# Optimization experiments

Measured on AMD Instinct MI355X. Metric: run time of the kernel, lower is better.

## Reference

```python
import jax, jax.numpy as jnp
import numpy as np

B, S, D, H = 8, 1024, 1024, 16
HD = D // H  # head_size = 64


def layernorm(x, g, b, eps=1e-5):
    mu = jnp.mean(x, axis=-1, keepdims=True)
    var = jnp.var(x, axis=-1, keepdims=True)
    return (x - mu) * jax.lax.rsqrt(var + eps) * g + b


def setup_inputs() -> dict:
    key = jax.random.key(0)
    ks = jax.random.split(key, 12)
    s_attn = 1.0 / np.sqrt(D)
    inp = {
        "x": jax.random.normal(ks[0], (B, S, D), dtype=jnp.float32),
        # per-head q/k/v projections (bias=False), stacked: [H, D, HD]
        "Wq": jax.random.normal(ks[1], (H, D, HD), dtype=jnp.float32) * s_attn,
        "Wk": jax.random.normal(ks[2], (H, D, HD), dtype=jnp.float32) * s_attn,
        "Wv": jax.random.normal(ks[3], (H, D, HD), dtype=jnp.float32) * s_attn,
        "Wo": jax.random.normal(ks[4], (D, D), dtype=jnp.float32) * s_attn,
        "bo": jnp.zeros((D,), dtype=jnp.float32),
        # FFN: hidden = 1 * n_embd (as in source)
        "W1": jax.random.normal(ks[5], (D, D), dtype=jnp.float32) * s_attn,
        "b1": jnp.zeros((D,), dtype=jnp.float32),
        "W2": jax.random.normal(ks[6], (D, D), dtype=jnp.float32) * s_attn,
        "b2": jnp.zeros((D,), dtype=jnp.float32),
        "g_ln1": jnp.ones((D,), dtype=jnp.float32),
        "b_ln1": jnp.zeros((D,), dtype=jnp.float32),
        "g_ln2": jnp.ones((D,), dtype=jnp.float32),
        "b_ln2": jnp.zeros((D,), dtype=jnp.float32),
    }
    return inp


def reference(x, Wq, Wk, Wv, Wo, bo, W1, b1, W2, b2, g_ln1, b_ln1, g_ln2, b_ln2):
    # pre-LN self-attention
    h = layernorm(x, g_ln1, b_ln1)
    q = jnp.einsum("bsd,hde->bhse", h, Wq)
    k = jnp.einsum("bsd,hde->bhse", h, Wk)
    v = jnp.einsum("bsd,hde->bhse", h, Wv)
    scale = HD ** -0.5  # k.shape[-1] ** -0.5
    wei = jax.nn.softmax(jnp.einsum("bhse,bhte->bhst", q, k) * scale, axis=-1)
    attn = jnp.einsum("bhst,bhte->bhse", wei, v)  # [B,H,S,HD]
    # concat heads (head order matches torch.cat over head list)
    attn = attn.transpose(0, 2, 1, 3).reshape(B, S, D)
    sa = attn @ Wo + bo
    x = x + sa
    # pre-LN FFN with exact GELU (torch nn.GELU default)
    h2 = layernorm(x, g_ln2, b_ln2)
    ff = jax.nn.gelu(h2 @ W1 + b1, approximate=False) @ W2 + b2
    return x + ff
```

## Files before the change

kernel.cpp:

```cpp
#include <hip/hip_runtime.h>
#include <hip/hip_bf16.h>
#include <math.h>

#define B_ 8
#define S_ 1024
#define D_ 1024
#define H_ 16
#define HD_ 64

typedef __bf16 bf16x8 __attribute__((ext_vector_type(8)));
typedef __bf16 bf16x4 __attribute__((ext_vector_type(4)));
typedef float f32x4 __attribute__((ext_vector_type(4)));

__device__ __forceinline__ void gld_lds16(const __bf16* g, __bf16* l) {
  __builtin_amdgcn_global_load_lds(
      (const __attribute__((address_space(1))) void*)g,
      (__attribute__((address_space(3))) void*)l, 16, 0, 0);
}

__global__ __launch_bounds__(256) void ln_kernel(const float* __restrict__ x,
                                                 const float* __restrict__ g,
                                                 const float* __restrict__ b,
                                                 __bf16* __restrict__ out) {
  int row = blockIdx.x;
  const float* xr = x + (size_t)row * D_;
  __bf16* outr = out + (size_t)row * D_;
  int tid = threadIdx.x;

  float4 v = ((const float4*)xr)[tid];
  float s = v.x + v.y + v.z + v.w;
  float ss = v.x * v.x + v.y * v.y + v.z * v.z + v.w * v.w;

  #pragma unroll
  for (int m = 1; m < 64; m <<= 1) {
    s += __shfl_xor(s, m);
    ss += __shfl_xor(ss, m);
  }
  __shared__ float red[10];
  int wid = tid >> 6;
  if ((tid & 63) == 0) { red[wid] = s; red[4 + wid] = ss; }
  __syncthreads();
  if (tid == 0) {
    float ts = red[0] + red[1] + red[2] + red[3];
    float tss = red[4] + red[5] + red[6] + red[7];
    float mu = ts * (1.0f / D_);
    float var = tss * (1.0f / D_) - mu * mu;
    red[8] = mu;
    red[9] = rsqrtf(var + 1e-5f);
  }
  __syncthreads();
  float mu = red[8], rstd = red[9];
  float4 gv = ((const float4*)g)[tid];
  float4 bv = ((const float4*)b)[tid];
  bf16x4 o;
  o[0] = (__bf16)((v.x - mu) * rstd * gv.x + bv.x);
  o[1] = (__bf16)((v.y - mu) * rstd * gv.y + bv.y);
  o[2] = (__bf16)((v.z - mu) * rstd * gv.z + bv.z);
  o[3] = (__bf16)((v.w - mu) * rstd * gv.w + bv.w);
  *(bf16x4*)(outr + tid * 4) = o;
}

__global__ __launch_bounds__(256) void transpose_w(const float* __restrict__ in,
                                                   __bf16* __restrict__ out) {
  __shared__ float t[64][65];
  const int n0 = blockIdx.x * 64, k0 = blockIdx.y * 64;
  const int tid = threadIdx.x;
  const int r = tid >> 4, c4 = (tid & 15) * 4;
  #pragma unroll
  for (int i = 0; i < 4; ++i) {
    float4 v = *(const float4*)&in[(size_t)(k0 + i * 16 + r) * D_ + n0 + c4];
    t[i * 16 + r][c4 + 0] = v.x;
    t[i * 16 + r][c4 + 1] = v.y;
    t[i * 16 + r][c4 + 2] = v.z;
    t[i * 16 + r][c4 + 3] = v.w;
  }
  __syncthreads();
  #pragma unroll
  for (int i = 0; i < 4; ++i) {
    bf16x4 o;
    #pragma unroll
    for (int j = 0; j < 4; ++j) o[j] = (__bf16)t[c4 + j][i * 16 + r];
    *(bf16x4*)&out[(size_t)(n0 + i * 16 + r) * D_ + k0 + c4] = o;
  }
}

__global__ __launch_bounds__(256) void transpose_qkv(const float* __restrict__ Wq,
                                                     const float* __restrict__ Wk,
                                                     const float* __restrict__ Wv,
                                                     __bf16* __restrict__ out) {
  __shared__ float t[64][65];
  const int d0 = blockIdx.x * 64;
  const int h = blockIdx.y;
  const int which = blockIdx.z;
  const float* in = (which == 0 ? Wq : which == 1 ? Wk : Wv) + (size_t)h * D_ * HD_;
  const int tid = threadIdx.x;
  const int r = tid >> 4, c4 = (tid & 15) * 4;
  #pragma unroll
  for (int i = 0; i < 4; ++i) {
    float4 v = *(const float4*)&in[(size_t)(d0 + i * 16 + r) * HD_ + c4];
    t[i * 16 + r][c4 + 0] = v.x;
    t[i * 16 + r][c4 + 1] = v.y;
    t[i * 16 + r][c4 + 2] = v.z;
    t[i * 16 + r][c4 + 3] = v.w;
  }
  __syncthreads();
  #pragma unroll
  for (int i = 0; i < 4; ++i) {
    bf16x4 o;
    #pragma unroll
    for (int j = 0; j < 4; ++j) o[j] = (__bf16)t[c4 + j][i * 16 + r];
    *(bf16x4*)&out[(size_t)(which * 1024 + h * 64 + i * 16 + r) * D_ + d0 + c4] = o;
  }
}

#define MODE_QKV 0
#define MODE_PROJ 1
#define MODE_FF1 2
#define MODE_FF2 3

template <int MODE>
__global__ __launch_bounds__(256) void gemm_mfma(const __bf16* __restrict__ A,
                                                 const __bf16* __restrict__ Bt,
                                                 const float* __restrict__ bias,
                                                 const float* __restrict__ resid,
                                                 float* __restrict__ outf,
                                                 __bf16* __restrict__ outb,
                                                 int M, int N, int K) {
  __shared__ __align__(16) __bf16 As[128 * 64];
  __shared__ __align__(16) __bf16 Bs[128 * 64];
  const int tid = threadIdx.x;

  const int gx = (int)gridDim.x;
  const int nwg = gx * (int)gridDim.y;
  const int flat = (int)blockIdx.y * gx + (int)blockIdx.x;
  const int wg = (flat & 7) * (nwg >> 3) + (flat >> 3);
  const int m0 = (wg / gx) * 128, n0 = (wg % gx) * 128;

  const int w = tid >> 6, l = tid & 63, lr = l & 15, lg = l >> 4;
  const int wm = (w >> 1) * 64, wn = (w & 1) * 64;

  f32x4 acc[4][4] = {};

  for (int k0 = 0; k0 < K; k0 += 64) {
    __syncthreads();
    #pragma unroll
    for (int i = 0; i < 4; ++i) {
      int e = i * 256 + tid;
      int row = e >> 3;
      int col = ((e & 7) ^ (row & 7)) * 8;
      gld_lds16(A + (size_t)(m0 + row) * K + k0 + col, &As[e * 8]);
    }
    #pragma unroll
    for (int i = 0; i < 4; ++i) {
      int e = i * 256 + tid;
      int row = e >> 3;
      int col = ((e & 7) ^ (row & 7)) * 8;
      gld_lds16(Bt + (size_t)(n0 + row) * K + k0 + col, &Bs[e * 8]);
    }
    asm volatile("s_waitcnt vmcnt(0)");
    __syncthreads();

    #pragma unroll
    for (int kk = 0; kk < 2; ++kk) {
      bf16x8 af[4], bfr[4];
      #pragma unroll
      for (int i = 0; i < 4; ++i)
        af[i] = *(const bf16x8*)
            &As[((wm + i * 16 + lr) * 8 + ((kk * 4 + lg) ^ (lr & 7))) * 8];
      #pragma unroll
      for (int j = 0; j < 4; ++j)
        bfr[j] = *(const bf16x8*)
            &Bs[((wn + j * 16 + lr) * 8 + ((kk * 4 + lg) ^ (lr & 7))) * 8];
      #pragma unroll
      for (int i = 0; i < 4; ++i)
        #pragma unroll
        for (int j = 0; j < 4; ++j)
          acc[i][j] = __builtin_amdgcn_mfma_f32_16x16x32_bf16(af[i], bfr[j], acc[i][j], 0, 0, 0);
    }
  }

  #pragma unroll
  for (int i = 0; i < 4; ++i) {
    #pragma unroll
    for (int j = 0; j < 4; ++j) {
      #pragma unroll
      for (int r = 0; r < 4; ++r) {
        int m = m0 + wm + i * 16 + 4 * lg + r;
        int n = n0 + wn + j * 16 + lr;
        float val = acc[i][j][r];
        if (MODE == MODE_QKV) {
          int b = m >> 10, s = m & 1023;
          int which = n >> 10, hh = (n >> 6) & 15, e = n & 63;
          outb[(size_t)which * 8388608 + ((size_t)(b * 16 + hh) * 1024 + s) * 64 + e] =
              (__bf16)val;
        } else if (MODE == MODE_PROJ) {
          size_t idx = (size_t)m * 1024 + n;
          outf[idx] = resid[idx] + val + bias[n];
        } else if (MODE == MODE_FF1) {
          val += bias[n];
          outb[(size_t)m * 1024 + n] =
              (__bf16)(0.5f * val * (1.0f + erff(val * 0.70710678118654752f)));
        } else {
          size_t idx = (size_t)m * 1024 + n;
          outf[idx] = outf[idx] + val + bias[n];
        }
      }
    }
  }
}

__global__ __launch_bounds__(512) void fattn(const __bf16* __restrict__ q,
                                             const __bf16* __restrict__ k,
                                             const __bf16* __restrict__ v,
                                             __bf16* __restrict__ outC) {
  __shared__ __align__(16) __bf16 Klds[2][64 * 64];
  __shared__ __align__(16) __bf16 Vp[2][64][72];

  const int bid = blockIdx.x;
  const int bh = (bid & 7) * 16 + ((bid >> 3) & 15);
  const int qt = bid >> 7;
  const int tid = threadIdx.x;
  const int w = tid >> 6, l = tid & 63;
  const int lr = l & 15, lg = l >> 4;

  const size_t base = (size_t)bh * (S_ * HD_);
  const int qrow0 = qt * 128 + w * 16;
  const __bf16* kg = k + base;
  const __bf16* vg = v + base;

  const int krow = tid >> 3;
  const int kcol = ((tid & 7) ^ (krow & 7)) * 8;
  const int vc = (l & 0x20) + ((l & 0xC) << 1) + ((l & 0x10) >> 2) + (l & 3);

  bf16x8 qf0, qf1;
  {
    const __bf16* qp = q + base + (size_t)(qrow0 + lr) * HD_ + lg * 8;
    qf0 = *(const bf16x8*)(qp);
    qf1 = *(const bf16x8*)(qp + 32);
    #pragma unroll
    for (int i = 0; i < 8; ++i) qf0[i] = (__bf16)((float)qf0[i] * 0.125f);
    #pragma unroll
    for (int i = 0; i < 8; ++i) qf1[i] = (__bf16)((float)qf1[i] * 0.125f);
  }

  f32x4 oacc[4] = {{0,0,0,0},{0,0,0,0},{0,0,0,0},{0,0,0,0}};
  float m_run = -1e30f, l_run = 0.f;

  gld_lds16(kg + (size_t)krow * HD_ + kcol, &Klds[0][tid * 8]);
  bf16x8 vr0, vr1;
  if (w < 4) {
    const __bf16* vp = vg + (size_t)l * HD_ + w * 16;
    vr0 = *(const bf16x8*)vp;
    vr1 = *(const bf16x8*)(vp + 8);
    #pragma unroll
    for (int i = 0; i < 8; ++i) Vp[0][w * 16 + i][vc] = vr0[i];
    #pragma unroll
    for (int i = 0; i < 8; ++i) Vp[0][w * 16 + 8 + i][vc] = vr1[i];
    const __bf16* vp1 = vg + (size_t)(64 + l) * HD_ + w * 16;
    vr0 = *(const bf16x8*)vp1;
    vr1 = *(const bf16x8*)(vp1 + 8);
  }
  asm volatile("s_waitcnt vmcnt(0)");
  __syncthreads();

  int cur = 0;
  for (int t = 0; t < 16; ++t) {
    {
      int tn = (t < 15) ? (t + 1) : 15;
      gld_lds16(kg + ((size_t)tn * 64 + krow) * HD_ + kcol, &Klds[cur ^ 1][tid * 8]);
    }

    f32x4 sacc[4];
    const __bf16* kb = &Klds[cur][0];
    __builtin_amdgcn_s_setprio(1);
    #pragma unroll
    for (int g = 0; g < 4; ++g) {
      bf16x8 kf0 = *(const bf16x8*)&kb[((16 * g + lr) * 8 + (lg ^ (lr & 7))) * 8];
      bf16x8 kf1 = *(const bf16x8*)&kb[((16 * g + lr) * 8 + ((lg + 4) ^ (lr & 7))) * 8];
      f32x4 z = {0.f, 0.f, 0.f, 0.f};
      z = __builtin_amdgcn_mfma_f32_16x16x32_bf16(kf0, qf0, z, 0, 0, 0);
      sacc[g] = __builtin_amdgcn_mfma_f32_16x16x32_bf16(kf1, qf1, z, 0, 0, 0);
    }
    __builtin_amdgcn_s_setprio(0);

    float tm = sacc[0][0];
    #pragma unroll
    for (int g = 0; g < 4; ++g)
      #pragma unroll
      for (int r = 0; r < 4; ++r) tm = fmaxf(tm, sacc[g][r]);
    tm = fmaxf(tm, __shfl_xor(tm, 16));
    tm = fmaxf(tm, __shfl_xor(tm, 32));

    if (!__all(tm - m_run <= 8.0f)) {
      float mn = fmaxf(m_run, tm);
      float corr = __expf(m_run - mn);
      m_run = mn;
      l_run *= corr;
      #pragma unroll
      for (int r = 0; r < 4; ++r) {
        float cq = __shfl(corr, 4 * lg + r);
        #pragma unroll
        for (int g = 0; g < 4; ++g) oacc[g][r] *= cq;
      }
    }

    float p[4][4];
    float ps = 0.f;
    #pragma unroll
    for (int g = 0; g < 4; ++g)
      #pragma unroll
      for (int r = 0; r < 4; ++r) {
        p[g][r] = __expf(sacc[g][r] - m_run);
        ps += p[g][r];
      }
    ps += __shfl_xor(ps, 16);
    ps += __shfl_xor(ps, 32);
    l_run += ps;

    if (w < 4) {
      #pragma unroll
      for (int i = 0; i < 8; ++i) Vp[cur ^ 1][w * 16 + i][vc] = vr0[i];
      #pragma unroll
      for (int i = 0; i < 8; ++i) Vp[cur ^ 1][w * 16 + 8 + i][vc] = vr1[i];
      int tnn = (t < 14) ? (t + 2) : 15;
      const __bf16* vp = vg + ((size_t)tnn * 64 + l) * HD_ + w * 16;
      vr0 = *(const bf16x8*)vp;
      vr1 = *(const bf16x8*)(vp + 8);
    }

    bf16x8 af0, af1;
    #pragma unroll
    for (int j = 0; j < 8; ++j) {
      af0[j] = (__bf16)p[j >> 2][j & 3];
      af1[j] = (__bf16)p[2 + (j >> 2)][j & 3];
    }
    __builtin_amdgcn_s_setprio(1);
    #pragma unroll
    for (int g = 0; g < 4; ++g) {
      bf16x8 vf0 = *(const bf16x8*)&Vp[cur][16 * g + lr][lg * 8];
      bf16x8 vf1 = *(const bf16x8*)&Vp[cur][16 * g + lr][32 + lg * 8];
      oacc[g] = __builtin_amdgcn_mfma_f32_16x16x32_bf16(af0, vf0, oacc[g], 0, 0, 0);
      oacc[g] = __builtin_amdgcn_mfma_f32_16x16x32_bf16(af1, vf1, oacc[g], 0, 0, 0);
    }
    __builtin_amdgcn_s_setprio(0);

    asm volatile("s_waitcnt vmcnt(0)");
    __syncthreads();
    cur ^= 1;
  }

  const int b = bh >> 4, hh = bh & 15;
  #pragma unroll
  for (int r = 0; r < 4; ++r) {
    float linv = 1.0f / __shfl(l_run, 4 * lg + r);
    int srow = qrow0 + 4 * lg + r;
    __bf16* op = outC + ((size_t)(b * S_ + srow)) * D_ + hh * HD_;
    #pragma unroll
    for (int g = 0; g < 4; ++g) op[16 * g + lr] = (__bf16)(oacc[g][r] * linv);
  }
}

extern "C" void kernel_launch(void* const* d_in, const int* in_sizes, int n_in,
                              void* d_out, int out_size, void* d_ws, size_t ws_size,
                              hipStream_t stream) {
  const float* x   = (const float*)d_in[0];
  const float* Wq  = (const float*)d_in[1];
  const float* Wk  = (const float*)d_in[2];
  const float* Wv  = (const float*)d_in[3];
  const float* Wo  = (const float*)d_in[4];
  const float* bo  = (const float*)d_in[5];
  const float* W1  = (const float*)d_in[6];
  const float* b1  = (const float*)d_in[7];
  const float* W2  = (const float*)d_in[8];
  const float* b2  = (const float*)d_in[9];
  const float* g1  = (const float*)d_in[10];
  const float* bl1 = (const float*)d_in[11];
  const float* g2  = (const float*)d_in[12];
  const float* bl2 = (const float*)d_in[13];
  float* out = (float*)d_out;

  const size_t MN = (size_t)B_ * S_ * D_;
  __bf16* h     = (__bf16*)d_ws;
  __bf16* wt    = h + MN;
  __bf16* qkv   = wt + (size_t)6144 * 1024;
  __bf16* attnC = qkv + 3 * MN;
  __bf16* ff1   = attnC + MN;

  __bf16* wqkv_t = wt;
  __bf16* wo_t   = wt + (size_t)3072 * 1024;
  __bf16* w1_t   = wt + (size_t)4096 * 1024;
  __bf16* w2_t   = wt + (size_t)5120 * 1024;

  const int rows = B_ * S_;

  ln_kernel<<<rows, 256, 0, stream>>>(x, g1, bl1, h);
  transpose_qkv<<<dim3(16, 16, 3), 256, 0, stream>>>(Wq, Wk, Wv, wqkv_t);
  transpose_w<<<dim3(16, 16), 256, 0, stream>>>(Wo, wo_t);
  transpose_w<<<dim3(16, 16), 256, 0, stream>>>(W1, w1_t);
  transpose_w<<<dim3(16, 16), 256, 0, stream>>>(W2, w2_t);

  gemm_mfma<MODE_QKV><<<dim3(24, 64), 256, 0, stream>>>(
      h, wqkv_t, nullptr, nullptr, nullptr, qkv, rows, 3072, D_);
  fattn<<<1024, 512, 0, stream>>>(qkv, qkv + MN, qkv + 2 * MN, attnC);
  gemm_mfma<MODE_PROJ><<<dim3(8, 64), 256, 0, stream>>>(
      attnC, wo_t, bo, x, out, nullptr, rows, D_, D_);
  ln_kernel<<<rows, 256, 0, stream>>>(out, g2, bl2, h);
  gemm_mfma<MODE_FF1><<<dim3(8, 64), 256, 0, stream>>>(
      h, w1_t, b1, nullptr, nullptr, ff1, rows, D_, D_);
  gemm_mfma<MODE_FF2><<<dim3(8, 64), 256, 0, stream>>>(
      ff1, w2_t, b2, nullptr, out, nullptr, rows, D_, D_);
}
```

Measured before the change: 254.4 us.

## Merge weight transposes, fold softmax scale into QKV, compute row sums via MFMA

Replaces four weight-transpose launches with a single kernel over six matrices. The attention scale and log2(e) are folded into the Q projection epilogue so the attention kernel can use exp2f and skip rescaling Q. The softmax denominator now comes from an extra MFMA against a ones vector instead of shuffle reductions, and the rescale threshold is raised. V staging uses all 8 waves with an XOR-swizzled LDS layout instead of a padded one, which removes a register buffer. These cut launch overhead and VALU/shuffle work in the attention loop, at the cost of two extra MFMAs per tile and the row sum being built from bf16-rounded probabilities.

```diff
diff --git a/kernel.cpp b/kernel.cpp
--- a/kernel.cpp
+++ b/kernel.cpp
@@ -11,6 +11,8 @@
 typedef __bf16 bf16x8 __attribute__((ext_vector_type(8)));
 typedef __bf16 bf16x4 __attribute__((ext_vector_type(4)));
 typedef float f32x4 __attribute__((ext_vector_type(4)));
+
+#define FMAX3(a, b, c) fmaxf(fmaxf((a), (b)), (c))
 
 __device__ __forceinline__ void gld_lds16(const __bf16* g, __bf16* l) {
   __builtin_amdgcn_global_load_lds(
@@ -60,15 +62,37 @@
   *(bf16x4*)(outr + tid * 4) = o;
 }
 
-__global__ __launch_bounds__(256) void transpose_w(const float* __restrict__ in,
-                                                   __bf16* __restrict__ out) {
+__global__ __launch_bounds__(256) void transpose_all(const float* __restrict__ Wq,
+                                                     const float* __restrict__ Wk,
+                                                     const float* __restrict__ Wv,
+                                                     const float* __restrict__ Wo,
+                                                     const float* __restrict__ W1,
+                                                     const float* __restrict__ W2,
+                                                     __bf16* __restrict__ out) {
   __shared__ float t[64][65];
-  const int n0 = blockIdx.x * 64, k0 = blockIdx.y * 64;
+  const int x = blockIdx.x, y = blockIdx.y, z = blockIdx.z;
   const int tid = threadIdx.x;
   const int r = tid >> 4, c4 = (tid & 15) * 4;
+
+  const float* src;
+  int stride, orowbase, kbase;
+  if (z < 3) {
+    const float* W = (z == 0 ? Wq : z == 1 ? Wk : Wv);
+    src = W + (size_t)y * (D_ * HD_) + (size_t)(x * 64) * HD_;
+    stride = HD_;
+    orowbase = z * 1024 + y * 64;
+    kbase = x * 64;
+  } else {
+    const float* W = (z == 3 ? Wo : z == 4 ? W1 : W2);
+    src = W + (size_t)(y * 64) * D_ + x * 64;
+    stride = D_;
+    orowbase = z * 1024 + x * 64;
+    kbase = y * 64;
+  }
+
   #pragma unroll
   for (int i = 0; i < 4; ++i) {
-    float4 v = *(const float4*)&in[(size_t)(k0 + i * 16 + r) * D_ + n0 + c4];
+    float4 v = *(const float4*)&src[(size_t)(i * 16 + r) * stride + c4];
     t[i * 16 + r][c4 + 0] = v.x;
     t[i * 16 + r][c4 + 1] = v.y;
     t[i * 16 + r][c4 + 2] = v.z;
@@ -80,36 +104,7 @@
     bf16x4 o;
     #pragma unroll
     for (int j = 0; j < 4; ++j) o[j] = (__bf16)t[c4 + j][i * 16 + r];
-    *(bf16x4*)&out[(size_t)(n0 + i * 16 + r) * D_ + k0 + c4] = o;
-  }
-}
-
-__global__ __launch_bounds__(256) void transpose_qkv(const float* __restrict__ Wq,
-                                                     const float* __restrict__ Wk,
-                                                     const float* __restrict__ Wv,
-                                                     __bf16* __restrict__ out) {
-  __shared__ float t[64][65];
-  const int d0 = blockIdx.x * 64;
-  const int h = blockIdx.y;
-  const int which = blockIdx.z;
-  const float* in = (which == 0 ? Wq : which == 1 ? Wk : Wv) + (size_t)h * D_ * HD_;
-  const int tid = threadIdx.x;
-  const int r = tid >> 4, c4 = (tid & 15) * 4;
-  #pragma unroll
-  for (int i = 0; i < 4; ++i) {
-    float4 v = *(const float4*)&in[(size_t)(d0 + i * 16 + r) * HD_ + c4];
-    t[i * 16 + r][c4 + 0] = v.x;
-    t[i * 16 + r][c4 + 1] = v.y;
-    t[i * 16 + r][c4 + 2] = v.z;
-    t[i * 16 + r][c4 + 3] = v.w;
-  }
-  __syncthreads();
-  #pragma unroll
-  for (int i = 0; i < 4; ++i) {
-    bf16x4 o;
-    #pragma unroll
-    for (int j = 0; j < 4; ++j) o[j] = (__bf16)t[c4 + j][i * 16 + r];
-    *(bf16x4*)&out[(size_t)(which * 1024 + h * 64 + i * 16 + r) * D_ + d0 + c4] = o;
+    *(bf16x4*)&out[(size_t)(orowbase + i * 16 + r) * 1024 + kbase + c4] = o;
   }
 }
 
@@ -117,6 +112,8 @@
 #define MODE_PROJ 1
 #define MODE_FF1 2
 #define MODE_FF2 3
+
+#define QSCALE 0.18033688011112042f
 
 template <int MODE>
 __global__ __launch_bounds__(256) void gemm_mfma(const __bf16* __restrict__ A,
@@ -191,6 +188,7 @@
         if (MODE == MODE_QKV) {
           int b = m >> 10, s = m & 1023;
           int which = n >> 10, hh = (n >> 6) & 15, e = n & 63;
+          if (which == 0) val *= QSCALE;
           outb[(size_t)which * 8388608 + ((size_t)(b * 16 + hh) * 1024 + s) * 64 + e] =
               (__bf16)val;
         } else if (MODE == MODE_PROJ) {
@@ -214,7 +212,7 @@
                                              const __bf16* __restrict__ v,
                                              __bf16* __restrict__ outC) {
   __shared__ __align__(16) __bf16 Klds[2][64 * 64];
-  __shared__ __align__(16) __bf16 Vp[2][64][72];
+  __shared__ __align__(16) __bf16 Vp[2][64 * 64];
 
   const int bid = blockIdx.x;
   const int bh = (bid & 7) * 16 + ((bid >> 3) & 15);
@@ -231,34 +229,29 @@
   const int krow = tid >> 3;
   const int kcol = ((tid & 7) ^ (krow & 7)) * 8;
   const int vc = (l & 0x20) + ((l & 0xC) << 1) + ((l & 0x10) >> 2) + (l & 3);
+  const int vchi = vc >> 3, vclo = vc & 7;
 
   bf16x8 qf0, qf1;
   {
     const __bf16* qp = q + base + (size_t)(qrow0 + lr) * HD_ + lg * 8;
     qf0 = *(const bf16x8*)(qp);
     qf1 = *(const bf16x8*)(qp + 32);
-    #pragma unroll
-    for (int i = 0; i < 8; ++i) qf0[i] = (__bf16)((float)qf0[i] * 0.125f);
-    #pragma unroll
-    for (int i = 0; i < 8; ++i) qf1[i] = (__bf16)((float)qf1[i] * 0.125f);
-  }
-
-  f32x4 oacc[4] = {{0,0,0,0},{0,0,0,0},{0,0,0,0},{0,0,0,0}};
-  float m_run = -1e30f, l_run = 0.f;
+  }
+
+  const __bf16 onev = (lr == 0) ? (__bf16)1.0f : (__bf16)0.0f;
+  const bf16x8 vones = {onev, onev, onev, onev, onev, onev, onev, onev};
+
+  f32x4 oacc[5] = {};
+  float m_run = -1e30f;
 
   gld_lds16(kg + (size_t)krow * HD_ + kcol, &Klds[0][tid * 8]);
-  bf16x8 vr0, vr1;
-  if (w < 4) {
-    const __bf16* vp = vg + (size_t)l * HD_ + w * 16;
-    vr0 = *(const bf16x8*)vp;
-    vr1 = *(const bf16x8*)(vp + 8);
-    #pragma unroll
-    for (int i = 0; i < 8; ++i) Vp[0][w * 16 + i][vc] = vr0[i];
-    #pragma unroll
-    for (int i = 0; i < 8; ++i) Vp[0][w * 16 + 8 + i][vc] = vr1[i];
-    const __bf16* vp1 = vg + (size_t)(64 + l) * HD_ + w * 16;
-    vr0 = *(const bf16x8*)vp1;
-    vr1 = *(const bf16x8*)(vp1 + 8);
+  bf16x8 vr;
+  {
+    vr = *(const bf16x8*)(vg + (size_t)l * HD_ + w * 8);
+    #pragma unroll
+    for (int i = 0; i < 8; ++i)
+      Vp[0][(w * 8 + i) * 64 + ((vchi ^ i) << 3) + vclo] = vr[i];
+    vr = *(const bf16x8*)(vg + (size_t)(64 + l) * HD_ + w * 8);
   }
   asm volatile("s_waitcnt vmcnt(0)");
   __syncthreads();
@@ -283,49 +276,38 @@
     }
     __builtin_amdgcn_s_setprio(0);
 
-    float tm = sacc[0][0];
-    #pragma unroll
-    for (int g = 0; g < 4; ++g)
-      #pragma unroll
-      for (int r = 0; r < 4; ++r) tm = fmaxf(tm, sacc[g][r]);
+    float m0 = FMAX3(sacc[0][0], sacc[0][1], sacc[0][2]);
+    float m1 = FMAX3(sacc[0][3], sacc[1][0], sacc[1][1]);
+    float m2 = FMAX3(sacc[1][2], sacc[1][3], sacc[2][0]);
+    float m3 = FMAX3(sacc[2][1], sacc[2][2], sacc[2][3]);
+    float m4 = FMAX3(sacc[3][0], sacc[3][1], sacc[3][2]);
+    float tm = FMAX3(FMAX3(m0, m1, m2), FMAX3(m3, m4, sacc[3][3]), m_run);
     tm = fmaxf(tm, __shfl_xor(tm, 16));
     tm = fmaxf(tm, __shfl_xor(tm, 32));
 
-    if (!__all(tm - m_run <= 8.0f)) {
-      float mn = fmaxf(m_run, tm);
-      float corr = __expf(m_run - mn);
-      m_run = mn;
-      l_run *= corr;
+    if (!__all(tm - m_run <= 11.5f)) {
+      float corr = exp2f(m_run - tm);
+      m_run = tm;
       #pragma unroll
       for (int r = 0; r < 4; ++r) {
         float cq = __shfl(corr, 4 * lg + r);
         #pragma unroll
-        for (int g = 0; g < 4; ++g) oacc[g][r] *= cq;
+        for (int g = 0; g < 5; ++g) oacc[g][r] *= cq;
       }
     }
 
     float p[4][4];
-    float ps = 0.f;
     #pragma unroll
     for (int g = 0; g < 4; ++g)
       #pragma unroll
-      for (int r = 0; r < 4; ++r) {
-        p[g][r] = __expf(sacc[g][r] - m_run);
-        ps += p[g][r];
-      }
-    ps += __shfl_xor(ps, 16);
-    ps += __shfl_xor(ps, 32);
-    l_run += ps;
-
-    if (w < 4) {
-      #pragma unroll
-      for (int i = 0; i < 8; ++i) Vp[cur ^ 1][w * 16 + i][vc] = vr0[i];
-      #pragma unroll
-      for (int i = 0; i < 8; ++i) Vp[cur ^ 1][w * 16 + 8 + i][vc] = vr1[i];
+      for (int r = 0; r < 4; ++r) p[g][r] = exp2f(sacc[g][r] - m_run);
+
+    #pragma unroll
+    for (int i = 0; i < 8; ++i)
+      Vp[cur ^ 1][(w * 8 + i) * 64 + ((vchi ^ i) << 3) + vclo] = vr[i];
+    {
       int tnn = (t < 14) ? (t + 2) : 15;
-      const __bf16* vp = vg + ((size_t)tnn * 64 + l) * HD_ + w * 16;
-      vr0 = *(const bf16x8*)vp;
-      vr1 = *(const bf16x8*)(vp + 8);
+      vr = *(const bf16x8*)(vg + ((size_t)tnn * 64 + l) * HD_ + w * 8);
     }
 
     bf16x8 af0, af1;
@@ -337,11 +319,13 @@
     __builtin_amdgcn_s_setprio(1);
     #pragma unroll
     for (int g = 0; g < 4; ++g) {
-      bf16x8 vf0 = *(const bf16x8*)&Vp[cur][16 * g + lr][lg * 8];
-      bf16x8 vf1 = *(const bf16x8*)&Vp[cur][16 * g + lr][32 + lg * 8];
+      bf16x8 vf0 = *(const bf16x8*)&Vp[cur][(16 * g + lr) * 64 + ((lg ^ (lr & 7)) << 3)];
+      bf16x8 vf1 = *(const bf16x8*)&Vp[cur][(16 * g + lr) * 64 + (((lg + 4) ^ (lr & 7)) << 3)];
       oacc[g] = __builtin_amdgcn_mfma_f32_16x16x32_bf16(af0, vf0, oacc[g], 0, 0, 0);
       oacc[g] = __builtin_amdgcn_mfma_f32_16x16x32_bf16(af1, vf1, oacc[g], 0, 0, 0);
     }
+    oacc[4] = __builtin_amdgcn_mfma_f32_16x16x32_bf16(af0, vones, oacc[4], 0, 0, 0);
+    oacc[4] = __builtin_amdgcn_mfma_f32_16x16x32_bf16(af1, vones, oacc[4], 0, 0, 0);
     __builtin_amdgcn_s_setprio(0);
 
     asm volatile("s_waitcnt vmcnt(0)");
@@ -352,7 +336,7 @@
   const int b = bh >> 4, hh = bh & 15;
   #pragma unroll
   for (int r = 0; r < 4; ++r) {
-    float linv = 1.0f / __shfl(l_run, 4 * lg + r);
+    float linv = 1.0f / __shfl(oacc[4][r], l & 48);
     int srow = qrow0 + 4 * lg + r;
     __bf16* op = outC + ((size_t)(b * S_ + srow)) * D_ + hh * HD_;
     #pragma unroll
@@ -394,10 +378,7 @@
   const int rows = B_ * S_;
 
   ln_kernel<<<rows, 256, 0, stream>>>(x, g1, bl1, h);
-  transpose_qkv<<<dim3(16, 16, 3), 256, 0, stream>>>(Wq, Wk, Wv, wqkv_t);
-  transpose_w<<<dim3(16, 16), 256, 0, stream>>>(Wo, wo_t);
-  transpose_w<<<dim3(16, 16), 256, 0, stream>>>(W1, w1_t);
-  transpose_w<<<dim3(16, 16), 256, 0, stream>>>(W2, w2_t);
+  transpose_all<<<dim3(16, 16, 6), 256, 0, stream>>>(Wq, Wk, Wv, Wo, W1, W2, wt);
 
   gemm_mfma<MODE_QKV><<<dim3(24, 64), 256, 0, stream>>>(
       h, wqkv_t, nullptr, nullptr, nullptr, qkv, rows, 3072, D_);
```

Result: no change. 253.1 us (-0.5%).
